# Kernel tuning notes

Hardware: AMD Instinct MI355X
Metric: run time of the kernel (lower is better)

The kernel has to match this reference:

```python
import jax, jax.numpy as jnp
import numpy as np

N, D_IN, D_HID, D_OUT, E = 100000, 128, 256, 64, 1600000


def setup_inputs() -> dict:
    key = jax.random.key(0)
    ks = jax.random.split(key, 6)
    x = jax.random.normal(ks[0], (N, D_IN), dtype=jnp.float32)
    edge_index = jax.random.randint(ks[1], (2, E), 0, N, dtype=jnp.int64)
    # Linear params (PyTorch convention: y = x @ W.T + b)
    W1 = jax.random.normal(ks[2], (D_HID, D_IN), dtype=jnp.float32) / np.sqrt(D_IN)
    b1 = jax.random.normal(ks[3], (D_HID,), dtype=jnp.float32) * 0.01
    W2 = jax.random.normal(ks[4], (D_OUT, D_HID), dtype=jnp.float32) / np.sqrt(D_HID)
    b2 = jax.random.normal(ks[5], (D_OUT,), dtype=jnp.float32) * 0.01
    return {"x": x, "edge_index": edge_index, "W1": W1, "b1": b1, "W2": W2, "b2": b2}


def _scatter_mean(vals, dst, num_nodes):
    # sum neighbor features per destination node, divide by in-degree (0-degree -> 0)
    s = jax.ops.segment_sum(vals, dst, num_segments=num_nodes)
    cnt = jax.ops.segment_sum(jnp.ones((dst.shape[0],), vals.dtype), dst, num_segments=num_nodes)
    return s / jnp.maximum(cnt, 1.0)[:, None]


def _sage_layer(x, src, dst, W, b):
    neighbors = x[src]                      # [E, d] gather
    agg = _scatter_mean(neighbors, dst, x.shape[0])  # [N, d]
    return agg @ W.T + b


def reference(x, edge_index, W1, b1, W2, b2):
    src, dst = edge_index[0], edge_index[1]
    h = _sage_layer(x, src, dst, W1, b1)
    h = jax.nn.relu(h)
    # dropout is identity at inference (training=False)
    y = _sage_layer(h, src, dst, W2, b2)
    return jax.nn.log_softmax(y, axis=1)
```

## Files before the change

### kernel.cpp

```cpp
#include <hip/hip_runtime.h>


typedef __attribute__((ext_vector_type(8))) short bf16x8;
typedef __attribute__((ext_vector_type(4))) float f32x4;
typedef __attribute__((ext_vector_type(2))) float f32x2;

#define BSHIFT 10
#define BMASK  1023
#define SRCMASK 0x1FFFF
#define TBIN   4096

#if __has_builtin(__builtin_amdgcn_cvt_pk_f32_fp8) && __has_builtin(__builtin_amdgcn_cvt_pk_fp8_f32)
#define HAVE_FP8_CVT 1
#else
#define HAVE_FP8_CVT 0
#endif

__device__ inline ushort f2bf(float f) {
  union { float f; unsigned u; } c; c.f = f;
  unsigned r = (c.u + 0x7fffu + ((c.u >> 16) & 1u)) >> 16;
  return (ushort)r;
}
__device__ inline float bf2f(ushort u) {
  union { unsigned u; float f; } c; c.u = ((unsigned)u) << 16;
  return c.f;
}

#if HAVE_FP8_CVT
template <bool HI>
__device__ inline f32x2 fp8x2f(unsigned w) {
  return __builtin_amdgcn_cvt_pk_f32_fp8((int)w, HI);
}
template <bool HI>
__device__ inline unsigned fp8pack2(unsigned old, float a, float b) {
  return (unsigned)__builtin_amdgcn_cvt_pk_fp8_f32(a, b, (int)old, HI);
}
#else
__device__ inline float fp8tof_1(unsigned b) {
  unsigned e = (b >> 3) & 15u, m = b & 7u;
  float v;
  if (e == 0) v = (float)m * 0x1p-9f;
  else { union { unsigned u; float f; } c; c.u = ((e + 120u) << 23) | (m << 20); v = c.f; }
  return (b & 0x80u) ? -v : v;
}
template <bool HI>
__device__ inline f32x2 fp8x2f(unsigned w) {
  unsigned sh = HI ? 16 : 0;
  f32x2 r;
  r.x = fp8tof_1((w >> sh) & 0xFFu);
  r.y = fp8tof_1((w >> (sh + 8)) & 0xFFu);
  return r;
}
__device__ inline unsigned f2fp8_1(float f) {
  float af = fabsf(f);
  unsigned s = (f < 0.f) ? 0x80u : 0u;
  if (!(af < 448.f)) return s | 0x7Eu;
  if (af < 0x1p-6f) {
    int m = (int)rintf(af * 512.0f);
    if (m >= 8) return s | 0x08u;
    return s | (unsigned)m;
  }
  int e;
  frexpf(af, &e);
  int E = e - 1;
  int q = (int)rintf(ldexpf(af, 3 - E));
  if (q >= 16) { q = 8; E += 1; if (E > 8) return s | 0x7Eu; }
  return s | ((unsigned)(E + 7) << 3) | ((unsigned)q & 7u);
}
template <bool HI>
__device__ inline unsigned fp8pack2(unsigned old, float a, float b) {
  unsigned pair = f2fp8_1(a) | (f2fp8_1(b) << 8);
  return HI ? ((old & 0x0000FFFFu) | (pair << 16)) : ((old & 0xFFFF0000u) | pair);
}
#endif

__global__ void __launch_bounds__(64) k_detect(const int* __restrict__ ei, int* __restrict__ flag) {
  int t = threadIdx.x;
  int v = ei[2 * t + 1];
  unsigned long long m = __ballot(v != 0);
  if (t == 0) *flag = (m == 0ull) ? 1 : 0;
}

__global__ void __launch_bounds__(256) k_prep_x(const float4* __restrict__ x4, uint2* __restrict__ xq8, int total8) {
  int i = blockIdx.x * 256 + threadIdx.x;
  if (i >= total8) return;
  float4 v0 = x4[2 * i], v1 = x4[2 * i + 1];
  unsigned w0 = fp8pack2<false>(0u, v0.x, v0.y);
  w0 = fp8pack2<true>(w0, v0.z, v0.w);
  unsigned w1 = fp8pack2<false>(0u, v1.x, v1.y);
  w1 = fp8pack2<true>(w1, v1.z, v1.w);
  xq8[i] = make_uint2(w0, w1);
}

__global__ void __launch_bounds__(256) k_prep_w(const float* __restrict__ W1, const float* __restrict__ W2,
                                                ushort* __restrict__ W1f, ushort* __restrict__ W2f) {
  int idx = blockIdx.x * 256 + threadIdx.x;
  if (idx < 32768) {
    int jt = idx >> 11, rem = idx & 2047;
    int kt = rem >> 9, rem2 = rem & 511;
    int l = rem2 >> 3, e = rem2 & 7;
    int k = kt * 32 + (l >> 4) * 8 + e;
    int j = jt * 16 + (l & 15);
    W1f[idx] = f2bf(W1[j * 128 + k]);
  } else {
    int i2 = idx - 32768;
    if (i2 < 16384) {
      int ot = i2 >> 12, rem = i2 & 4095;
      int kt = rem >> 9;
      int l = (rem >> 3) & 63, e = rem & 7;
      int k = kt * 32 + (l >> 4) * 8 + e;
      int o = ot * 16 + (l & 15);
      W2f[i2] = f2bf(W2[o * 256 + k]);
    }
  }
}

__global__ void __launch_bounds__(256) k_bhist(const int* __restrict__ ei, const int* __restrict__ flag,
                                               int* __restrict__ bcnt, int E, int NB) {
  __shared__ int h[128];
  int t = threadIdx.x;
  if (t < 128) h[t] = 0;
  __syncthreads();
  bool f64 = (*flag != 0);
  int stride = gridDim.x * 256;
  for (int e = blockIdx.x * 256 + t; e < E; e += stride) {
    int d;
    if (f64) d = (int)((const long long*)ei)[(size_t)E + e];
    else     d = ei[(size_t)E + e];
    atomicAdd(&h[d >> BSHIFT], 1);
  }
  __syncthreads();
  if (t < NB && h[t]) atomicAdd(&bcnt[t], h[t]);
}

__global__ void __launch_bounds__(128) k_bscan(const int* __restrict__ bcnt, int* __restrict__ bbase,
                                               int* __restrict__ bcur, int* __restrict__ row_ptr,
                                               int NB, int N, int E) {
  __shared__ int s[128];
  int t = threadIdx.x;
  int v = (t < NB) ? bcnt[t] : 0;
  s[t] = v;
  __syncthreads();
  for (int o = 1; o < 128; o <<= 1) {
    int u = (t >= o) ? s[t - o] : 0;
    __syncthreads();
    s[t] += u;
    __syncthreads();
  }
  if (t < NB) {
    int base = s[t] - v;
    bbase[t] = base;
    bcur[t] = base;
  }
  if (t == 0) {
    bbase[NB] = E;
    row_ptr[N] = E;
  }
}

__global__ void __launch_bounds__(256) k_bin(const int* __restrict__ ei, const int* __restrict__ flag,
                                             int* __restrict__ bcur, int* __restrict__ gpair, int E, int NB) {
  __shared__ int hist[128], base[128], segb[128], cur[128], scanb[128];
  __shared__ int ent[TBIN];
  __shared__ int gdx[TBIN];
  int t = threadIdx.x;
  int e0 = blockIdx.x * TBIN;
  int cnt = E - e0; if (cnt > TBIN) cnt = TBIN;
  if (t < 128) hist[t] = 0;
  __syncthreads();
  bool f64 = (*flag != 0);
  int ment[16], mbk[16];
#pragma unroll
  for (int i = 0; i < 16; ++i) {
    int idx = t + i * 256;
    mbk[i] = -1;
    if (idx < cnt) {
      int e = e0 + idx;
      int s, d;
      if (f64) {
        const long long* p = (const long long*)ei;
        s = (int)p[e];
        d = (int)p[(size_t)E + e];
      } else {
        s = ei[e];
        d = ei[(size_t)E + e];
      }
      int b = d >> BSHIFT;
      mbk[i] = b;
      ment[i] = ((d & BMASK) << 17) | s;
      atomicAdd(&hist[b], 1);
    }
  }
  __syncthreads();
  if (t < 128) scanb[t] = hist[t];
  __syncthreads();
  for (int o = 1; o < 128; o <<= 1) {
    int u = 0;
    if (t < 128 && t >= o) u = scanb[t - o];
    __syncthreads();
    if (t < 128) scanb[t] += u;
    __syncthreads();
  }
  if (t < 128) {
    int b0 = scanb[t] - hist[t];
    base[t] = b0;
    cur[t] = b0;
    segb[t] = (t < NB && hist[t] > 0) ? atomicAdd(&bcur[t], hist[t]) : 0;
  }
  __syncthreads();
#pragma unroll
  for (int i = 0; i < 16; ++i) {
    int b = mbk[i];
    if (b >= 0) {
      int pos = atomicAdd(&cur[b], 1);
      ent[pos] = ment[i];
      gdx[pos] = segb[b] + (pos - base[b]);
    }
  }
  __syncthreads();
  for (int i = t; i < cnt; i += 256) gpair[gdx[i]] = ent[i];
}

__global__ void __launch_bounds__(1024) k_bcsr(const int* __restrict__ gpair, const int* __restrict__ bbase,
                                               int* __restrict__ row_ptr, float* __restrict__ inv_deg,
                                               int* __restrict__ csr, int N) {
  __shared__ int hist[1024], pre[1024], cur[1024];
  int b = blockIdx.x, t = threadIdx.x;
  int start = bbase[b], end = bbase[b + 1];
  hist[t] = 0;
  __syncthreads();
  for (int i = start + t; i < end; i += 1024) {
    int e = gpair[i];
    atomicAdd(&hist[e >> 17], 1);
  }
  __syncthreads();
  pre[t] = hist[t];
  __syncthreads();
  for (int o = 1; o < 1024; o <<= 1) {
    int u = (t >= o) ? pre[t - o] : 0;
    __syncthreads();
    pre[t] += u;
    __syncthreads();
  }
  int gbase = start + pre[t] - hist[t];
  int n = (b << BSHIFT) + t;
  if (n < N) {
    row_ptr[n] = gbase;
    inv_deg[n] = 1.0f / (float)(hist[t] > 0 ? hist[t] : 1);
  }
  cur[t] = gbase;
  __syncthreads();
  for (int i = start + t; i < end; i += 1024) {
    int e = gpair[i];
    int pos = atomicAdd(&cur[e >> 17], 1);
    csr[pos] = e & SRCMASK;
  }
}

__global__ void __launch_bounds__(256) k_agg1(const unsigned char* __restrict__ xq, const int* __restrict__ csr,
                                              const int* __restrict__ row_ptr, const float* __restrict__ inv_deg,
                                              ushort* __restrict__ agg1b, int N) {
  const int lane = threadIdx.x & 63;
  const int g = lane >> 4, p = lane & 15;
  const int n0 = (blockIdx.x * 4 + (threadIdx.x >> 6)) * 4;
  if (n0 >= N) return;
  const int n = n0 + g;
  int rpidx = n0 + (lane < 4 ? lane : 4);
  if (rpidx > N) rpidx = N;
  const int rv = row_ptr[rpidx];
  const int s = __shfl(rv, g);
  const int cnt = __shfl(rv, g + 1) - s;
  const float inv = inv_deg[n < N ? n : 0];
  int maxc = cnt;
  maxc = max(maxc, __shfl_xor(maxc, 16));
  maxc = max(maxc, __shfl_xor(maxc, 32));

  f32x2 a0 = (f32x2)(0.f), a1 = (f32x2)(0.f), a2 = (f32x2)(0.f), a3 = (f32x2)(0.f);
  for (int base = 0; base < maxc; base += 16) {
    int li = base + p, cm = cnt - 1;
    if (li > cm) li = cm;
    if (li < 0) li = 0;
    int ci = 0;
    if (cnt > 0) ci = csr[s + li];
#pragma unroll
    for (int u = 0; u < 8; ++u) {
      int idx = __shfl(ci, (lane & 48) + u);
      uint2 wv = *(const uint2*)(xq + (size_t)idx * 128 + p * 8);
      if (base + u >= cnt) { wv.x = 0u; wv.y = 0u; }
      a0 += fp8x2f<false>(wv.x); a1 += fp8x2f<true>(wv.x);
      a2 += fp8x2f<false>(wv.y); a3 += fp8x2f<true>(wv.y);
    }
    if (base + 8 < maxc) {
#pragma unroll
      for (int u = 8; u < 16; ++u) {
        int idx = __shfl(ci, (lane & 48) + u);
        uint2 wv = *(const uint2*)(xq + (size_t)idx * 128 + p * 8);
        if (base + u >= cnt) { wv.x = 0u; wv.y = 0u; }
        a0 += fp8x2f<false>(wv.x); a1 += fp8x2f<true>(wv.x);
        a2 += fp8x2f<false>(wv.y); a3 += fp8x2f<true>(wv.y);
      }
    }
  }
  if (n < N) {
    bf16x8 o;
    o[0] = (short)f2bf(a0.x * inv); o[1] = (short)f2bf(a0.y * inv);
    o[2] = (short)f2bf(a1.x * inv); o[3] = (short)f2bf(a1.y * inv);
    o[4] = (short)f2bf(a2.x * inv); o[5] = (short)f2bf(a2.y * inv);
    o[6] = (short)f2bf(a3.x * inv); o[7] = (short)f2bf(a3.y * inv);
    *(bf16x8*)(agg1b + (size_t)n * 128 + p * 8) = o;
  }
}

__global__ void __launch_bounds__(256) k_mlp(const ushort* __restrict__ agg1b, const bf16x8* __restrict__ w1f,
                                             const float* __restrict__ b1, const bf16x8* __restrict__ w2f,
                                             unsigned char* __restrict__ gq, int N) {
  __shared__ __align__(16) ushort sm[16896];
  ushort* aT = sm;
  ushort* hT = sm;
  const int t = threadIdx.x;
  const int n0 = blockIdx.x * 64;

#pragma unroll
  for (int i = 0; i < 4; ++i) {
    int idx = i * 256 + t;
    int row = idx >> 4, c8 = idx & 15;
    int rr = n0 + row; if (rr >= N) rr = N - 1;
    bf16x8 v = *(const bf16x8*)(agg1b + (size_t)rr * 128 + c8 * 8);
    *(bf16x8*)(aT + row * 136 + c8 * 8) = v;
  }
  __syncthreads();

  const int w = t >> 6, l = t & 63;
  const int lm = l & 15, lq = l >> 4;

  f32x4 acc[4][4];
#pragma unroll
  for (int mt = 0; mt < 4; ++mt)
#pragma unroll
    for (int nt = 0; nt < 4; ++nt) acc[mt][nt] = (f32x4)(0.f);

#pragma unroll
  for (int kt = 0; kt < 4; ++kt) {
    bf16x8 b[4], a[4];
#pragma unroll
    for (int nt = 0; nt < 4; ++nt)
      b[nt] = w1f[((w * 4 + nt) * 4 + kt) * 64 + l];
#pragma unroll
    for (int mt = 0; mt < 4; ++mt)
      a[mt] = *(const bf16x8*)(aT + (mt * 16 + lm) * 136 + kt * 32 + lq * 8);
#pragma unroll
    for (int mt = 0; mt < 4; ++mt)
#pragma unroll
      for (int nt = 0; nt < 4; ++nt)
        acc[mt][nt] = __builtin_amdgcn_mfma_f32_16x16x32_bf16(a[mt], b[nt], acc[mt][nt], 0, 0, 0);
  }
  __syncthreads();

#pragma unroll
  for (int nt = 0; nt < 4; ++nt) {
    int col = w * 64 + nt * 16 + lm;
    float bb = b1[col];
#pragma unroll
    for (int mt = 0; mt < 4; ++mt)
#pragma unroll
      for (int r = 0; r < 4; ++r) {
        int row = mt * 16 + lq * 4 + r;
        float hv = acc[mt][nt][r] + bb;
        hT[row * 264 + col] = f2bf(fmaxf(hv, 0.f));
      }
  }
  __syncthreads();

  f32x4 acc2[4];
#pragma unroll
  for (int ot = 0; ot < 4; ++ot) acc2[ot] = (f32x4)(0.f);
#pragma unroll
  for (int kt = 0; kt < 8; ++kt) {
    bf16x8 a2 = *(const bf16x8*)(hT + (w * 16 + lm) * 264 + kt * 32 + lq * 8);
#pragma unroll
    for (int ot = 0; ot < 4; ++ot) {
      bf16x8 bf = w2f[(ot * 8 + kt) * 64 + l];
      acc2[ot] = __builtin_amdgcn_mfma_f32_16x16x32_bf16(a2, bf, acc2[ot], 0, 0, 0);
    }
  }
#pragma unroll
  for (int ot = 0; ot < 4; ++ot)
#pragma unroll
    for (int r = 0; r < 4; ++r) {
      int row = n0 + w * 16 + lq * 4 + r;
      if (row < N) {
        unsigned pw = fp8pack2<false>(0u, acc2[ot][r], acc2[ot][r]);
        gq[(size_t)row * 64 + ot * 16 + lm] = (unsigned char)(pw & 0xFFu);
      }
    }
}

__global__ void __launch_bounds__(256) k_agg2(const unsigned char* __restrict__ gq, const int* __restrict__ csr,
                                              const int* __restrict__ row_ptr, const float* __restrict__ inv_deg,
                                              const float* __restrict__ b2, float* __restrict__ out, int N) {
  const int lane = threadIdx.x & 63;
  const int g = lane >> 4, p = lane & 15;
  const int n0 = (blockIdx.x * 4 + (threadIdx.x >> 6)) * 4;
  if (n0 >= N) return;
  const int n = n0 + g;
  int rpidx = n0 + (lane < 4 ? lane : 4);
  if (rpidx > N) rpidx = N;
  const int rv = row_ptr[rpidx];
  const int s = __shfl(rv, g);
  const int cnt = __shfl(rv, g + 1) - s;
  const float inv = inv_deg[n < N ? n : 0];
  const float4 bv = *(const float4*)(b2 + p * 4);
  int maxc = cnt;
  maxc = max(maxc, __shfl_xor(maxc, 16));
  maxc = max(maxc, __shfl_xor(maxc, 32));

  f32x2 a0 = (f32x2)(0.f), a1 = (f32x2)(0.f);
  for (int base = 0; base < maxc; base += 16) {
    int li = base + p, cm = cnt - 1;
    if (li > cm) li = cm;
    if (li < 0) li = 0;
    int ci = 0;
    if (cnt > 0) ci = csr[s + li];
#pragma unroll
    for (int u = 0; u < 8; ++u) {
      int idx = __shfl(ci, (lane & 48) + u);
      unsigned wv = *(const unsigned*)(gq + (size_t)idx * 64 + p * 4);
      if (base + u >= cnt) wv = 0u;
      a0 += fp8x2f<false>(wv); a1 += fp8x2f<true>(wv);
    }
    if (base + 8 < maxc) {
#pragma unroll
      for (int u = 8; u < 16; ++u) {
        int idx = __shfl(ci, (lane & 48) + u);
        unsigned wv = *(const unsigned*)(gq + (size_t)idx * 64 + p * 4);
        if (base + u >= cnt) wv = 0u;
        a0 += fp8x2f<false>(wv); a1 += fp8x2f<true>(wv);
      }
    }
  }
  float vx = a0.x * inv + bv.x;
  float vy = a0.y * inv + bv.y;
  float vz = a1.x * inv + bv.z;
  float vw = a1.y * inv + bv.w;
  float mx = fmaxf(fmaxf(vx, vy), fmaxf(vz, vw));
#pragma unroll
  for (int off = 1; off <= 8; off <<= 1) mx = fmaxf(mx, __shfl_xor(mx, off));
  float se = expf(vx - mx) + expf(vy - mx) + expf(vz - mx) + expf(vw - mx);
#pragma unroll
  for (int off = 1; off <= 8; off <<= 1) se += __shfl_xor(se, off);
  float lse = mx + logf(se);
  if (n < N) {
    float4 o;
    o.x = vx - lse; o.y = vy - lse; o.z = vz - lse; o.w = vw - lse;
    *(float4*)(out + (size_t)n * 64 + p * 4) = o;
  }
}

extern "C" void kernel_launch(void* const* d_in, const int* in_sizes, int n_in,
                              void* d_out, int out_size, void* d_ws, size_t ws_size,
                              hipStream_t stream) {
  const float* x  = (const float*)d_in[0];
  const int*   ei = (const int*)d_in[1];
  const float* W1 = (const float*)d_in[2];
  const float* b1 = (const float*)d_in[3];
  const float* W2 = (const float*)d_in[4];
  const float* b2 = (const float*)d_in[5];
  float* out = (float*)d_out;
  const int N = in_sizes[0] / 128;
  const int E = in_sizes[1] / 2;
  const int NB = (N + BMASK) >> BSHIFT;

  char* base = (char*)d_ws;
  size_t off = 0;
  auto alloc = [&](size_t bytes) -> char* {
    char* p = base + off;
    off += (bytes + 255) & ~(size_t)255;
    return p;
  };
  int*    flag    = (int*)alloc(4);
  int*    bcnt    = (int*)alloc((size_t)NB * 4);
  int*    bbase   = (int*)alloc((size_t)(NB + 1) * 4);
  int*    bcur    = (int*)alloc((size_t)NB * 4);
  int*    gpair   = (int*)alloc((size_t)E * 4);
  int*    row_ptr = (int*)alloc((size_t)(N + 1) * 4);
  float*  inv_deg = (float*)alloc((size_t)N * 4);
  int*    csr     = (int*)alloc((size_t)E * 4);
  unsigned char* xq = (unsigned char*)alloc((size_t)N * 128);
  ushort* W1f     = (ushort*)alloc((size_t)32768 * 2);
  ushort* W2f     = (ushort*)alloc((size_t)16384 * 2);
  ushort* agg1b   = (ushort*)alloc((size_t)N * 128 * 2);
  unsigned char* gq = (unsigned char*)alloc((size_t)N * 64);
  (void)ws_size; (void)n_in; (void)out_size;

  hipMemsetAsync(bcnt, 0, (size_t)NB * 4, stream);
  k_detect<<<1, 64, 0, stream>>>(ei, flag);
  k_prep_x<<<(N * 16 + 255) / 256, 256, 0, stream>>>((const float4*)x, (uint2*)xq, N * 16);
  k_prep_w<<<192, 256, 0, stream>>>(W1, W2, W1f, W2f);
  k_bhist<<<512, 256, 0, stream>>>(ei, flag, bcnt, E, NB);
  k_bscan<<<1, 128, 0, stream>>>(bcnt, bbase, bcur, row_ptr, NB, N, E);
  k_bin<<<(E + TBIN - 1) / TBIN, 256, 0, stream>>>(ei, flag, bcur, gpair, E, NB);
  k_bcsr<<<NB, 1024, 0, stream>>>(gpair, bbase, row_ptr, inv_deg, csr, N);
  k_agg1<<<(N + 15) / 16, 256, 0, stream>>>(xq, csr, row_ptr, inv_deg, agg1b, N);
  k_mlp<<<(N + 63) / 64, 256, 0, stream>>>(agg1b, (const bf16x8*)W1f, b1, (const bf16x8*)W2f, gq, N);
  k_agg2<<<(N + 15) / 16, 256, 0, stream>>>(gq, csr, row_ptr, inv_deg, b2, out, N);
}
```

Baseline: 282.8 us.

## Widen gather loads, add zero pad row, persistent grid-stride aggregation kernels

```diff
diff --git a/kernel.cpp b/kernel.cpp
--- a/kernel.cpp
+++ b/kernel.cpp
@@ -20,10 +20,6 @@
   union { float f; unsigned u; } c; c.f = f;
   unsigned r = (c.u + 0x7fffu + ((c.u >> 16) & 1u)) >> 16;
   return (ushort)r;
-}
-__device__ inline float bf2f(ushort u) {
-  union { unsigned u; float f; } c; c.u = ((unsigned)u) << 16;
-  return c.f;
 }
 
 #if HAVE_FP8_CVT
@@ -74,11 +70,15 @@
 }
 #endif
 
-__global__ void __launch_bounds__(64) k_detect(const int* __restrict__ ei, int* __restrict__ flag) {
+__global__ void __launch_bounds__(64) k_detect(const int* __restrict__ ei, int* __restrict__ flag,
+                                               unsigned long long* __restrict__ xpad,
+                                               unsigned long long* __restrict__ gpad) {
   int t = threadIdx.x;
   int v = ei[2 * t + 1];
   unsigned long long m = __ballot(v != 0);
   if (t == 0) *flag = (m == 0ull) ? 1 : 0;
+  if (t < 16) xpad[t] = 0ull;
+  if (t < 8)  gpad[t] = 0ull;
 }
 
 __global__ void __launch_bounds__(256) k_prep_x(const float4* __restrict__ x4, uint2* __restrict__ xq8, int total8) {
@@ -261,53 +261,75 @@
                                               const int* __restrict__ row_ptr, const float* __restrict__ inv_deg,
                                               ushort* __restrict__ agg1b, int N) {
   const int lane = threadIdx.x & 63;
-  const int g = lane >> 4, p = lane & 15;
-  const int n0 = (blockIdx.x * 4 + (threadIdx.x >> 6)) * 4;
-  if (n0 >= N) return;
-  const int n = n0 + g;
-  int rpidx = n0 + (lane < 4 ? lane : 4);
-  if (rpidx > N) rpidx = N;
-  const int rv = row_ptr[rpidx];
-  const int s = __shfl(rv, g);
-  const int cnt = __shfl(rv, g + 1) - s;
-  const float inv = inv_deg[n < N ? n : 0];
-  int maxc = cnt;
-  maxc = max(maxc, __shfl_xor(maxc, 16));
-  maxc = max(maxc, __shfl_xor(maxc, 32));
-
-  f32x2 a0 = (f32x2)(0.f), a1 = (f32x2)(0.f), a2 = (f32x2)(0.f), a3 = (f32x2)(0.f);
-  for (int base = 0; base < maxc; base += 16) {
-    int li = base + p, cm = cnt - 1;
-    if (li > cm) li = cm;
-    if (li < 0) li = 0;
-    int ci = 0;
-    if (cnt > 0) ci = csr[s + li];
-#pragma unroll
-    for (int u = 0; u < 8; ++u) {
-      int idx = __shfl(ci, (lane & 48) + u);
-      uint2 wv = *(const uint2*)(xq + (size_t)idx * 128 + p * 8);
-      if (base + u >= cnt) { wv.x = 0u; wv.y = 0u; }
-      a0 += fp8x2f<false>(wv.x); a1 += fp8x2f<true>(wv.x);
-      a2 += fp8x2f<false>(wv.y); a3 += fp8x2f<true>(wv.y);
-    }
-    if (base + 8 < maxc) {
-#pragma unroll
-      for (int u = 8; u < 16; ++u) {
-        int idx = __shfl(ci, (lane & 48) + u);
-        uint2 wv = *(const uint2*)(xq + (size_t)idx * 128 + p * 8);
-        if (base + u >= cnt) { wv.x = 0u; wv.y = 0u; }
-        a0 += fp8x2f<false>(wv.x); a1 += fp8x2f<true>(wv.x);
-        a2 += fp8x2f<false>(wv.y); a3 += fp8x2f<true>(wv.y);
+  const int g = lane >> 4;
+  const int g16 = lane & 48;
+  const int p = lane & 15;
+  const int h = (lane >> 3) & 1;
+  const int c = lane & 7;
+  const unsigned coff = (unsigned)c * 16u;
+  const int shbase = g16 + h;
+
+  const int NQ = (N + 3) >> 2;
+  const int tw = gridDim.x * 4;
+  int quad = (blockIdx.x * 256 + threadIdx.x) >> 6;
+  if (quad >= NQ) return;
+  int rp = quad * 4 + (lane < 4 ? lane : 4);
+  if (rp > N) rp = N;
+  int rv = row_ptr[rp];
+
+  for (;;) {
+    const int qn = quad + tw;
+    int rvn = 0;
+    if (qn < NQ) {
+      int rpn = qn * 4 + (lane < 4 ? lane : 4);
+      if (rpn > N) rpn = N;
+      rvn = row_ptr[rpn];
+    }
+    const int n = quad * 4 + g;
+    const int s = __shfl(rv, g);
+    const int cnt = __shfl(rv, g + 1) - s;
+    int maxc = cnt;
+    maxc = max(maxc, __shfl_xor(maxc, 16));
+    maxc = max(maxc, __shfl_xor(maxc, 32));
+
+    f32x2 a[8];
+#pragma unroll
+    for (int i = 0; i < 8; ++i) a[i] = (f32x2)(0.f);
+
+    for (int base = 0; base < maxc; base += 16) {
+      int li = base + p;
+      int ci = (li < cnt) ? csr[s + li] : N;
+#pragma unroll
+      for (int u = 0; u < 8; ++u) {
+        int idx = __shfl(ci, shbase + 2 * u);
+        unsigned off = ((unsigned)idx << 7) + coff;
+        const uint4 wv = *(const uint4*)(xq + off);
+        a[0] += fp8x2f<false>(wv.x); a[1] += fp8x2f<true>(wv.x);
+        a[2] += fp8x2f<false>(wv.y); a[3] += fp8x2f<true>(wv.y);
+        a[4] += fp8x2f<false>(wv.z); a[5] += fp8x2f<true>(wv.z);
+        a[6] += fp8x2f<false>(wv.w); a[7] += fp8x2f<true>(wv.w);
       }
     }
-  }
-  if (n < N) {
-    bf16x8 o;
-    o[0] = (short)f2bf(a0.x * inv); o[1] = (short)f2bf(a0.y * inv);
-    o[2] = (short)f2bf(a1.x * inv); o[3] = (short)f2bf(a1.y * inv);
-    o[4] = (short)f2bf(a2.x * inv); o[5] = (short)f2bf(a2.y * inv);
-    o[6] = (short)f2bf(a3.x * inv); o[7] = (short)f2bf(a3.y * inv);
-    *(bf16x8*)(agg1b + (size_t)n * 128 + p * 8) = o;
+#pragma unroll
+    for (int i = 0; i < 8; ++i) {
+      a[i].x += __shfl_xor(a[i].x, 8);
+      a[i].y += __shfl_xor(a[i].y, 8);
+    }
+    if (n < N) {
+      const float inv = inv_deg[n];
+      bf16x8 o;
+#pragma unroll
+      for (int k = 0; k < 4; ++k) {
+        f32x2 v0 = a[k], v1 = a[k + 4];
+        float vx = h ? v1.x : v0.x;
+        float vy = h ? v1.y : v0.y;
+        o[2 * k]     = (short)f2bf(vx * inv);
+        o[2 * k + 1] = (short)f2bf(vy * inv);
+      }
+      *(bf16x8*)(agg1b + (size_t)n * 128 + c * 16 + h * 8) = o;
+    }
+    if (qn >= NQ) break;
+    quad = qn; rv = rvn;
   }
 }
 
@@ -399,60 +421,100 @@
                                               const int* __restrict__ row_ptr, const float* __restrict__ inv_deg,
                                               const float* __restrict__ b2, float* __restrict__ out, int N) {
   const int lane = threadIdx.x & 63;
-  const int g = lane >> 4, p = lane & 15;
-  const int n0 = (blockIdx.x * 4 + (threadIdx.x >> 6)) * 4;
-  if (n0 >= N) return;
-  const int n = n0 + g;
-  int rpidx = n0 + (lane < 4 ? lane : 4);
-  if (rpidx > N) rpidx = N;
-  const int rv = row_ptr[rpidx];
-  const int s = __shfl(rv, g);
-  const int cnt = __shfl(rv, g + 1) - s;
-  const float inv = inv_deg[n < N ? n : 0];
-  const float4 bv = *(const float4*)(b2 + p * 4);
-  int maxc = cnt;
-  maxc = max(maxc, __shfl_xor(maxc, 16));
-  maxc = max(maxc, __shfl_xor(maxc, 32));
-
-  f32x2 a0 = (f32x2)(0.f), a1 = (f32x2)(0.f);
-  for (int base = 0; base < maxc; base += 16) {
-    int li = base + p, cm = cnt - 1;
-    if (li > cm) li = cm;
-    if (li < 0) li = 0;
-    int ci = 0;
-    if (cnt > 0) ci = csr[s + li];
-#pragma unroll
-    for (int u = 0; u < 8; ++u) {
-      int idx = __shfl(ci, (lane & 48) + u);
-      unsigned wv = *(const unsigned*)(gq + (size_t)idx * 64 + p * 4);
-      if (base + u >= cnt) wv = 0u;
-      a0 += fp8x2f<false>(wv); a1 += fp8x2f<true>(wv);
-    }
-    if (base + 8 < maxc) {
-#pragma unroll
-      for (int u = 8; u < 16; ++u) {
-        int idx = __shfl(ci, (lane & 48) + u);
-        unsigned wv = *(const unsigned*)(gq + (size_t)idx * 64 + p * 4);
-        if (base + u >= cnt) wv = 0u;
-        a0 += fp8x2f<false>(wv); a1 += fp8x2f<true>(wv);
+  const int g = lane >> 4;
+  const int g16 = lane & 48;
+  const int p = lane & 15;
+  const int q2 = (lane >> 2) & 3;
+  const int c = lane & 3;
+  const unsigned coff = (unsigned)c * 16u;
+  const int shbase = g16 + q2;
+
+  const int NQ = (N + 3) >> 2;
+  const int tw = gridDim.x * 4;
+  int quad = (blockIdx.x * 256 + threadIdx.x) >> 6;
+  if (quad >= NQ) return;
+  int rp = quad * 4 + (lane < 4 ? lane : 4);
+  if (rp > N) rp = N;
+  int rv = row_ptr[rp];
+
+  float4 bv0 = *(const float4*)(b2 + c * 16);
+  float4 bv1 = *(const float4*)(b2 + c * 16 + 4);
+  float4 bv2 = *(const float4*)(b2 + c * 16 + 8);
+  float4 bv3 = *(const float4*)(b2 + c * 16 + 12);
+
+  for (;;) {
+    const int qn = quad + tw;
+    int rvn = 0;
+    if (qn < NQ) {
+      int rpn = qn * 4 + (lane < 4 ? lane : 4);
+      if (rpn > N) rpn = N;
+      rvn = row_ptr[rpn];
+    }
+    const int n = quad * 4 + g;
+    const int s = __shfl(rv, g);
+    const int cnt = __shfl(rv, g + 1) - s;
+    int maxc = cnt;
+    maxc = max(maxc, __shfl_xor(maxc, 16));
+    maxc = max(maxc, __shfl_xor(maxc, 32));
+
+    f32x2 a[8];
+#pragma unroll
+    for (int i = 0; i < 8; ++i) a[i] = (f32x2)(0.f);
+
+    for (int base = 0; base < maxc; base += 16) {
+      int li = base + p;
+      int ci = (li < cnt) ? csr[s + li] : N;
+#pragma unroll
+      for (int u = 0; u < 4; ++u) {
+        int idx = __shfl(ci, shbase + 4 * u);
+        unsigned off = ((unsigned)idx << 6) + coff;
+        const uint4 wv = *(const uint4*)(gq + off);
+        a[0] += fp8x2f<false>(wv.x); a[1] += fp8x2f<true>(wv.x);
+        a[2] += fp8x2f<false>(wv.y); a[3] += fp8x2f<true>(wv.y);
+        a[4] += fp8x2f<false>(wv.z); a[5] += fp8x2f<true>(wv.z);
+        a[6] += fp8x2f<false>(wv.w); a[7] += fp8x2f<true>(wv.w);
       }
     }
-  }
-  float vx = a0.x * inv + bv.x;
-  float vy = a0.y * inv + bv.y;
-  float vz = a1.x * inv + bv.z;
-  float vw = a1.y * inv + bv.w;
-  float mx = fmaxf(fmaxf(vx, vy), fmaxf(vz, vw));
-#pragma unroll
-  for (int off = 1; off <= 8; off <<= 1) mx = fmaxf(mx, __shfl_xor(mx, off));
-  float se = expf(vx - mx) + expf(vy - mx) + expf(vz - mx) + expf(vw - mx);
-#pragma unroll
-  for (int off = 1; off <= 8; off <<= 1) se += __shfl_xor(se, off);
-  float lse = mx + logf(se);
-  if (n < N) {
-    float4 o;
-    o.x = vx - lse; o.y = vy - lse; o.z = vz - lse; o.w = vw - lse;
-    *(float4*)(out + (size_t)n * 64 + p * 4) = o;
+#pragma unroll
+    for (int i = 0; i < 8; ++i) {
+      a[i].x += __shfl_xor(a[i].x, 4); a[i].y += __shfl_xor(a[i].y, 4);
+      a[i].x += __shfl_xor(a[i].x, 8); a[i].y += __shfl_xor(a[i].y, 8);
+    }
+    const float inv = inv_deg[n < N ? n : 0];
+    float v[16];
+    v[0]  = a[0].x * inv + bv0.x;  v[1]  = a[0].y * inv + bv0.y;
+    v[2]  = a[1].x * inv + bv0.z;  v[3]  = a[1].y * inv + bv0.w;
+    v[4]  = a[2].x * inv + bv1.x;  v[5]  = a[2].y * inv + bv1.y;
+    v[6]  = a[3].x * inv + bv1.z;  v[7]  = a[3].y * inv + bv1.w;
+    v[8]  = a[4].x * inv + bv2.x;  v[9]  = a[4].y * inv + bv2.y;
+    v[10] = a[5].x * inv + bv2.z;  v[11] = a[5].y * inv + bv2.w;
+    v[12] = a[6].x * inv + bv3.x;  v[13] = a[6].y * inv + bv3.y;
+    v[14] = a[7].x * inv + bv3.z;  v[15] = a[7].y * inv + bv3.w;
+    float mx = v[0];
+#pragma unroll
+    for (int j = 1; j < 16; ++j) mx = fmaxf(mx, v[j]);
+    mx = fmaxf(mx, __shfl_xor(mx, 1));
+    mx = fmaxf(mx, __shfl_xor(mx, 2));
+    float se = 0.f;
+#pragma unroll
+    for (int j = 0; j < 16; ++j) se += expf(v[j] - mx);
+    se += __shfl_xor(se, 1);
+    se += __shfl_xor(se, 2);
+    float lse = mx + logf(se);
+    if (n < N && q2 == 0) {
+      float* po = out + (size_t)n * 64 + c * 16;
+      float4 o0, o1, o2, o3;
+      o0.x = v[0] - lse;  o0.y = v[1] - lse;  o0.z = v[2] - lse;  o0.w = v[3] - lse;
+      o1.x = v[4] - lse;  o1.y = v[5] - lse;  o1.z = v[6] - lse;  o1.w = v[7] - lse;
+      o2.x = v[8] - lse;  o2.y = v[9] - lse;  o2.z = v[10] - lse; o2.w = v[11] - lse;
+      o3.x = v[12] - lse; o3.y = v[13] - lse; o3.z = v[14] - lse; o3.w = v[15] - lse;
+      *(float4*)(po)      = o0;
+      *(float4*)(po + 4)  = o1;
+      *(float4*)(po + 8)  = o2;
+      *(float4*)(po + 12) = o3;
+    }
+    if (qn >= NQ) break;
+    quad = qn; rv = rvn;
   }
 }
 
@@ -485,22 +547,24 @@
   int*    row_ptr = (int*)alloc((size_t)(N + 1) * 4);
   float*  inv_deg = (float*)alloc((size_t)N * 4);
   int*    csr     = (int*)alloc((size_t)E * 4);
-  unsigned char* xq = (unsigned char*)alloc((size_t)N * 128);
+  unsigned char* xq = (unsigned char*)alloc((size_t)(N + 1) * 128);
   ushort* W1f     = (ushort*)alloc((size_t)32768 * 2);
   ushort* W2f     = (ushort*)alloc((size_t)16384 * 2);
   ushort* agg1b   = (ushort*)alloc((size_t)N * 128 * 2);
-  unsigned char* gq = (unsigned char*)alloc((size_t)N * 64);
+  unsigned char* gq = (unsigned char*)alloc((size_t)(N + 1) * 64);
   (void)ws_size; (void)n_in; (void)out_size;
 
   hipMemsetAsync(bcnt, 0, (size_t)NB * 4, stream);
-  k_detect<<<1, 64, 0, stream>>>(ei, flag);
+  k_detect<<<1, 64, 0, stream>>>(ei, flag,
+                                 (unsigned long long*)(xq + (size_t)N * 128),
+                                 (unsigned long long*)(gq + (size_t)N * 64));
   k_prep_x<<<(N * 16 + 255) / 256, 256, 0, stream>>>((const float4*)x, (uint2*)xq, N * 16);
   k_prep_w<<<192, 256, 0, stream>>>(W1, W2, W1f, W2f);
   k_bhist<<<512, 256, 0, stream>>>(ei, flag, bcnt, E, NB);
   k_bscan<<<1, 128, 0, stream>>>(bcnt, bbase, bcur, row_ptr, NB, N, E);
   k_bin<<<(E + TBIN - 1) / TBIN, 256, 0, stream>>>(ei, flag, bcur, gpair, E, NB);
   k_bcsr<<<NB, 1024, 0, stream>>>(gpair, bbase, row_ptr, inv_deg, csr, N);
-  k_agg1<<<(N + 15) / 16, 256, 0, stream>>>(xq, csr, row_ptr, inv_deg, agg1b, N);
+  k_agg1<<<2048, 256, 0, stream>>>(xq, csr, row_ptr, inv_deg, agg1b, N);
   k_mlp<<<(N + 63) / 64, 256, 0, stream>>>(agg1b, (const bf16x8*)W1f, b1, (const bf16x8*)W2f, gq, N);
-  k_agg2<<<(N + 15) / 16, 256, 0, stream>>>(gq, csr, row_ptr, inv_deg, b2, out, N);
-}
+  k_agg2<<<2048, 256, 0, stream>>>(gq, csr, row_ptr, inv_deg, b2, out, N);
+}
```

Measured after the change: 272.3 us. 1.04x faster.
